# Kernel tuning notes

Hardware: AMD Instinct MI355X
Metric: run time of the kernel (lower is better)

## Reference

```python
import jax, jax.numpy as jnp
import numpy as np

N = 50000      # nodes
E = 800000     # random edges (self loops appended in reference)
B = 500        # graphs
H = 4          # attention heads
F = 64         # feature_dim (per-head out channels)
SLOPE = 0.2    # GATConv leaky_relu negative slope


def gat_layer(x, src, dst, W, att_s, att_d, b):
    # x: [N, Fin]; W: [Fin, H*F]; att_s/att_d: [H, F]; b: [H*F]
    h = (x @ W).reshape(N, H, F)                       # [N,H,F]
    a_s = jnp.einsum('nhf,hf->nh', h, att_s)           # [N,H]
    a_d = jnp.einsum('nhf,hf->nh', h, att_d)           # [N,H]
    e = jax.nn.leaky_relu(a_s[src] + a_d[dst], SLOPE)  # [E',H]
    emax = jax.ops.segment_max(e, dst, num_segments=N) # [N,H] (finite: self loops)
    ee = jnp.exp(e - emax[dst])
    denom = jax.ops.segment_sum(ee, dst, num_segments=N)
    alpha = ee / denom[dst]                            # [E',H]
    out = jax.ops.segment_sum(alpha[:, :, None] * h[src], dst, num_segments=N)
    return out.reshape(N, H * F) + b


def setup_inputs() -> dict:
    key = jax.random.key(0)
    ks = jax.random.split(key, 32)
    s = 0.05
    inp = {
        'node_features': jax.random.normal(ks[0], (N, 5), jnp.float32),
        'building_mask': jax.random.randint(ks[1], (N,), 0, 2),
        'batch': jnp.sort(jax.random.randint(ks[2], (N,), 0, B)),
        'edge_index': jax.random.randint(ks[3], (2, E), 0, N),
        'bbox_W': jax.random.normal(ks[4], (5, 64)) * s,
        'bbox_b': jnp.zeros((64,), jnp.float32),
        'mask_embed': jax.random.normal(ks[5], (2, 64)) * s,
        'node_W': jax.random.normal(ks[6], (128, 64)) * s,
        'node_b': jnp.zeros((64,), jnp.float32),
        'w0': jax.random.normal(ks[7], (64, 256)) * s,
        'as0': jax.random.normal(ks[8], (H, F)) * s,
        'ad0': jax.random.normal(ks[9], (H, F)) * s,
        'b0': jnp.zeros((256,), jnp.float32),
        'w1': jax.random.normal(ks[10], (256, 256)) * s,
        'as1': jax.random.normal(ks[11], (H, F)) * s,
        'ad1': jax.random.normal(ks[12], (H, F)) * s,
        'b1': jnp.zeros((256,), jnp.float32),
        'w2': jax.random.normal(ks[13], (256, 256)) * s,
        'as2': jax.random.normal(ks[14], (H, F)) * s,
        'ad2': jax.random.normal(ks[15], (H, F)) * s,
        'b2': jnp.zeros((256,), jnp.float32),
        'agg_W': jax.random.normal(ks[16], (832, 256)) * s,
        'agg_b': jnp.zeros((256,), jnp.float32),
        'mu_W': jax.random.normal(ks[17], (256, 256)) * s,
        'mu_b': jnp.zeros((256,), jnp.float32),
        'var_W': jax.random.normal(ks[18], (256, 256)) * s,
        'var_b': jnp.zeros((256,), jnp.float32),
    }
    return inp


def reference(node_features, building_mask, batch, edge_index,
              bbox_W, bbox_b, mask_embed, node_W, node_b,
              w0, as0, ad0, b0, w1, as1, ad1, b1, w2, as2, ad2, b2,
              agg_W, agg_b, mu_W, mu_b, var_W, var_b):
    # node featurization
    x = jax.nn.relu(node_features @ bbox_W + bbox_b)          # [N,64]
    m = jax.nn.relu(mask_embed[building_mask])                 # [N,64]
    n0 = jax.nn.relu(jnp.concatenate([x, m], -1) @ node_W + node_b)  # [N,64]

    # self loops (GATConv add_self_loops=True)
    loop = jnp.arange(N, dtype=edge_index.dtype)
    src = jnp.concatenate([edge_index[0], loop])
    dst = jnp.concatenate([edge_index[1], loop])

    g = jax.ops.segment_max(n0, batch, num_segments=B, indices_are_sorted=True)
    g_embed = [g]

    n_t = jax.nn.relu(gat_layer(n0, src, dst, w0, as0, ad0, b0))
    g_embed.append(jax.ops.segment_max(n_t, batch, num_segments=B, indices_are_sorted=True))

    for (W, a_s, a_d, b) in [(w1, as1, ad1, b1), (w2, as2, ad2, b2)]:
        n_t = jax.nn.relu(gat_layer(n_t, src, dst, W, a_s, a_d, b))
        g_embed.append(jax.ops.segment_max(n_t, batch, num_segments=B, indices_are_sorted=True))

    latent = jnp.concatenate(g_embed, -1) @ agg_W + agg_b      # [B,256]
    mu = latent @ mu_W + mu_b
    log_var = latent @ var_W + var_b
    return (mu, log_var)
```

## Files before the change

kernel.cpp:

```cpp
#include <hip/hip_runtime.h>

#define NN 50000
#define EE 800000
#define BB 500

typedef short v8s __attribute__((ext_vector_type(8)));
typedef float v4f __attribute__((ext_vector_type(4)));

__device__ __forceinline__ float bf2f(unsigned short u) {
    union { unsigned int i; float f; } v; v.i = ((unsigned int)u) << 16; return v.f;
}
__device__ __forceinline__ unsigned short f2bf(float f) {
    union { float f; unsigned int i; } v; v.f = f;
    unsigned int x = v.i;
    unsigned int r = (x + 0x7FFFu + ((x >> 16) & 1u)) >> 16;
    return (unsigned short)r;
}

__device__ __forceinline__ void gll16(const unsigned short* g, v8s* l) {
    __builtin_amdgcn_global_load_lds((const __attribute__((address_space(1))) unsigned int*)g,
                                     (__attribute__((address_space(3))) unsigned int*)l, 16, 0, 0);
}

__global__ void k_sentinel(float* out, float val) {
    int i = blockIdx.x * blockDim.x + threadIdx.x;
    if (i < BB * 512) out[i] = val;
}

__global__ void k_prep(const float* __restrict__ nf, const int* __restrict__ bmask,
                       const float* __restrict__ bboxW, const float* __restrict__ bboxb,
                       const float* __restrict__ membed, unsigned short* __restrict__ feat,
                       const float* __restrict__ a0, unsigned short* __restrict__ d0,
                       const float* __restrict__ a1, unsigned short* __restrict__ d1,
                       const float* __restrict__ a2, unsigned short* __restrict__ d2,
                       const float* __restrict__ a3, unsigned short* __restrict__ d3,
                       int* __restrict__ cur, float* __restrict__ gcat) {
    int g = blockIdx.x * blockDim.x + threadIdx.x;
    if (g < NN) cur[g] = 0;
    if (g < NN * 64) {
        int n = g >> 6, f = g & 63;
        float s = bboxb[f];
        for (int k = 0; k < 5; ++k) s += nf[n * 5 + k] * bboxW[k * 64 + f];
        s = fmaxf(s, 0.f);
        int bm = bmask[n]; if ((unsigned)bm > 1u) bm = 0;
        float mv = fmaxf(membed[bm * 64 + f], 0.f);
        feat[(size_t)n * 128 + f] = f2bf(s);
        feat[(size_t)n * 128 + 64 + f] = f2bf(mv);
        return;
    }
    g -= NN * 64;
    if (g >= 155648) {
        if (g < 155648 + BB * 832) {
            int idx = g - 155648;
            gcat[idx] = 0.f;
        }
        return;
    }
    const float* in; unsigned short* out; int K, Nout, idx;
    if (g < 8192)        { in = a0; out = d0; K = 128; Nout = 64;  idx = g; }
    else if (g < 24576)  { in = a1; out = d1; K = 64;  Nout = 256; idx = g - 8192; }
    else if (g < 90112)  { in = a2; out = d2; K = 256; Nout = 256; idx = g - 24576; }
    else                 { in = a3; out = d3; K = 256; Nout = 256; idx = g - 90112; }
    int k = idx / Nout, n = idx % Nout;
    out[n * K + k] = f2bf(in[idx]);
}

template <int KT, bool BR, bool ATT, int GY, bool GM>
__global__ __launch_bounds__(256) void k_gemm(const unsigned short* __restrict__ A,
                                              const unsigned short* __restrict__ Bt,
                                              const float* __restrict__ bias,
                                              unsigned short* __restrict__ C, int M, int ldc,
                                              const float* __restrict__ atts, const float* __restrict__ attd,
                                              float* __restrict__ asA, float* __restrict__ adA, int nbx,
                                              const int* __restrict__ batch, float* __restrict__ gmax) {
    constexpr int NT = KT / 64;
    constexpr int NB = (NT > 1) ? 2 : 1;
    __shared__ v8s As[NB][512];
    __shared__ v8s Bs[NB][512];
    __shared__ float ap[4][4][4][4][2];
    const int t = threadIdx.x;
    int bx, by;
    if (GY == 4) {
        int p = blockIdx.x;
        int gidx = p >> 5, r = p & 31;
        bx = gidx * 8 + (r & 7);
        by = r >> 3;
        if (bx >= nbx) return;
    } else {
        bx = blockIdx.x; by = 0;
    }
    const int m0 = bx * 64;
    const int n0g = by * 64;
    const int l = t & 63, w = t >> 6;
    const int q = l >> 4, r16 = l & 15;
    const int nloc = w * 16 + r16;

    const int roff0 = (w * 2 + 0) * 8 + (l >> 3);
    const int roff1 = (w * 2 + 1) * 8 + (l >> 3);
    const int kc = (l & 7) ^ (l >> 3);
    const unsigned short* Asrc0 = A + (size_t)(m0 + roff0) * KT + kc * 8;
    const unsigned short* Asrc1 = A + (size_t)(m0 + roff1) * KT + kc * 8;
    const unsigned short* Bsrc0 = Bt + (size_t)(n0g + roff0) * KT + kc * 8;
    const unsigned short* Bsrc1 = Bt + (size_t)(n0g + roff1) * KT + kc * 8;

    v4f acc[4];
#pragma unroll
    for (int i = 0; i < 4; ++i) acc[i] = (v4f){0.f, 0.f, 0.f, 0.f};

    gll16(Asrc0, &As[0][(w * 2 + 0) * 64]);
    gll16(Asrc1, &As[0][(w * 2 + 1) * 64]);
    gll16(Bsrc0, &Bs[0][(w * 2 + 0) * 64]);
    gll16(Bsrc1, &Bs[0][(w * 2 + 1) * 64]);
    __syncthreads();
#pragma unroll
    for (int kt = 0; kt < NT; ++kt) {
        const int b = kt & (NB - 1);
        if (kt + 1 < NT) {
            const int nb = (kt + 1) & (NB - 1);
            gll16(Asrc0 + (kt + 1) * 64, &As[nb][(w * 2 + 0) * 64]);
            gll16(Asrc1 + (kt + 1) * 64, &As[nb][(w * 2 + 1) * 64]);
            gll16(Bsrc0 + (kt + 1) * 64, &Bs[nb][(w * 2 + 0) * 64]);
            gll16(Bsrc1 + (kt + 1) * 64, &Bs[nb][(w * 2 + 1) * 64]);
        }
#pragma unroll
        for (int s = 0; s < 2; ++s) {
            int c = s * 4 + q;
            v8s bfr = Bs[b][nloc * 8 + (c ^ (nloc & 7))];
#pragma unroll
            for (int mt = 0; mt < 4; ++mt) {
                v8s afr = As[b][(mt * 16 + r16) * 8 + (c ^ (r16 & 7))];
                acc[mt] = __builtin_amdgcn_mfma_f32_16x16x32_bf16(afr, bfr, acc[mt], 0, 0, 0);
            }
        }
        __syncthreads();
    }

    const int col = n0g + nloc;
#pragma unroll
    for (int mt = 0; mt < 4; ++mt) {
#pragma unroll
        for (int r = 0; r < 4; ++r) {
            int row = m0 + mt * 16 + q * 4 + r;
            if (row < M) {
                float v = acc[mt][r];
                if (BR) v = fmaxf(v + bias[col], 0.f);
                C[(size_t)row * ldc + col] = f2bf(v);
                if (GM) atomicMax((int*)(gmax + (size_t)batch[row] * 832 + col), __float_as_int(v));
            }
        }
    }
    if (ATT) {
        float sa = atts[n0g + nloc];
        float da = attd[n0g + nloc];
        float rs[4][4], rd[4][4];
#pragma unroll
        for (int mt = 0; mt < 4; ++mt)
#pragma unroll
            for (int r = 0; r < 4; ++r) { rs[mt][r] = acc[mt][r] * sa; rd[mt][r] = acc[mt][r] * da; }
#pragma unroll
        for (int d = 1; d < 16; d <<= 1) {
#pragma unroll
            for (int mt = 0; mt < 4; ++mt)
#pragma unroll
                for (int r = 0; r < 4; ++r) {
                    rs[mt][r] += __shfl_xor(rs[mt][r], d, 64);
                    rd[mt][r] += __shfl_xor(rd[mt][r], d, 64);
                }
        }
        if (r16 == 0) {
#pragma unroll
            for (int mt = 0; mt < 4; ++mt)
#pragma unroll
                for (int r = 0; r < 4; ++r) { ap[w][q][mt][r][0] = rs[mt][r]; ap[w][q][mt][r][1] = rd[mt][r]; }
        }
        __syncthreads();
        if (t < 128) {
            int row = t >> 1, which = t & 1;
            int qq = (row >> 2) & 3, mtt = row >> 4, rr = row & 3;
            float s = ap[0][qq][mtt][rr][which] + ap[1][qq][mtt][rr][which] +
                      ap[2][qq][mtt][rr][which] + ap[3][qq][mtt][rr][which];
            if (m0 + row < M) (which ? adA : asA)[(m0 + row) * 4 + by] = s;
        }
    }
}

#define SCAT_K 256
__global__ __launch_bounds__(256) void k_scatter(const int* __restrict__ ei, int* __restrict__ cur,
                                                 unsigned short* __restrict__ csr) {
    const int p = blockIdx.x & 7;
    const int j = blockIdx.x >> 3;
    const int plo = p * (NN / 8), phi = plo + (NN / 8);
    const int TOT = EE + NN;
    const int chunk = (TOT + SCAT_K - 1) / SCAT_K;
    const int e1 = min((j + 1) * chunk, TOT);
    for (int e = j * chunk + (int)threadIdx.x; e < e1; e += 256) {
        int d = (e < EE) ? ei[EE + e] : (e - EE);
        if (d < plo || d >= phi) continue;
        int s = (e < EE) ? ei[e] : d;
        if ((unsigned)s >= (unsigned)NN) s = d;
        int pos = atomicAdd(&cur[d], 1);
        if (pos < 64) csr[d * 64 + pos] = (unsigned short)s;
    }
}

__global__ __launch_bounds__(256) void k_agg(const unsigned short* __restrict__ h,
                                             const float* __restrict__ asA, const float* __restrict__ adA,
                                             const int* __restrict__ cur, const unsigned short* __restrict__ csr,
                                             const float* __restrict__ bias,
                                             unsigned short* __restrict__ nout,
                                             const int* __restrict__ batch,
                                             float* __restrict__ gcat, int gbase) {
    __shared__ int   sL[4][64];
    __shared__ float wL[4][64][4];
    __shared__ float mx[4][256];
    __shared__ int   gb[4];
    const int nd4 = threadIdx.x >> 6;
    const int node = blockIdx.x * 4 + nd4;
    const int l = threadIdx.x & 63;
    const int hl = l >> 4, k16 = l & 15;
    const int o0 = node << 6;
    int deg = cur[node]; if (deg > 64) deg = 64;
    const float ad4 = adA[node * 4 + hl];
    float sm = 0.f;
    for (int k = k16; k < deg; k += 16) {
        int s = csr[o0 + k];
        if (hl == 0) sL[nd4][k] = s;
        float e = asA[s * 4 + hl] + ad4;
        e = e > 0.f ? e : 0.2f * e;
        float w = __expf(e);
        wL[nd4][k][hl] = w;
        sm += w;
    }
#pragma unroll
    for (int d = 1; d < 16; d <<= 1) sm += __shfl_xor(sm, d, 64);
    const float rden = 1.f / sm;
    __syncthreads();
    float a0 = 0.f, a1 = 0.f, a2 = 0.f, a3 = 0.f;
    const int c = l * 4;
    int k = 0;
    for (; k + 4 <= deg; k += 4) {
        int s0 = sL[nd4][k], s1 = sL[nd4][k + 1], s2 = sL[nd4][k + 2], s3 = sL[nd4][k + 3];
        float w0 = wL[nd4][k][hl], w1 = wL[nd4][k + 1][hl], w2 = wL[nd4][k + 2][hl], w3 = wL[nd4][k + 3][hl];
        ushort4 h0 = *(const ushort4*)(h + (size_t)s0 * 256 + c);
        ushort4 h1 = *(const ushort4*)(h + (size_t)s1 * 256 + c);
        ushort4 h2 = *(const ushort4*)(h + (size_t)s2 * 256 + c);
        ushort4 h3 = *(const ushort4*)(h + (size_t)s3 * 256 + c);
        a0 += w0 * bf2f(h0.x) + w1 * bf2f(h1.x) + w2 * bf2f(h2.x) + w3 * bf2f(h3.x);
        a1 += w0 * bf2f(h0.y) + w1 * bf2f(h1.y) + w2 * bf2f(h2.y) + w3 * bf2f(h3.y);
        a2 += w0 * bf2f(h0.z) + w1 * bf2f(h1.z) + w2 * bf2f(h2.z) + w3 * bf2f(h3.z);
        a3 += w0 * bf2f(h0.w) + w1 * bf2f(h1.w) + w2 * bf2f(h2.w) + w3 * bf2f(h3.w);
    }
    for (; k < deg; ++k) {
        int s = sL[nd4][k];
        float w = wL[nd4][k][hl];
        ushort4 hv = *(const ushort4*)(h + (size_t)s * 256 + c);
        a0 += w * bf2f(hv.x); a1 += w * bf2f(hv.y); a2 += w * bf2f(hv.z); a3 += w * bf2f(hv.w);
    }
    float4 bv = *(const float4*)(bias + c);
    float v0 = fmaxf(a0 * rden + bv.x, 0.f);
    float v1 = fmaxf(a1 * rden + bv.y, 0.f);
    float v2 = fmaxf(a2 * rden + bv.z, 0.f);
    float v3 = fmaxf(a3 * rden + bv.w, 0.f);
    ushort4 o;
    o.x = f2bf(v0); o.y = f2bf(v1); o.z = f2bf(v2); o.w = f2bf(v3);
    *(ushort4*)(nout + (size_t)node * 256 + c) = o;

    mx[nd4][c + 0] = v0; mx[nd4][c + 1] = v1; mx[nd4][c + 2] = v2; mx[nd4][c + 3] = v3;
    if (l == 0) gb[nd4] = batch[node];
    __syncthreads();
    const int t = threadIdx.x;
    if (gb[0] == gb[1] && gb[1] == gb[2] && gb[2] == gb[3]) {
        float m = fmaxf(fmaxf(mx[0][t], mx[1][t]), fmaxf(mx[2][t], mx[3][t]));
        atomicMax((int*)(gcat + gb[0] * 832 + gbase + t), __float_as_int(m));
    } else {
        int* g = (int*)(gcat + gb[nd4] * 832 + gbase);
        atomicMax(g + c + 0, __float_as_int(v0));
        atomicMax(g + c + 1, __float_as_int(v1));
        atomicMax(g + c + 2, __float_as_int(v2));
        atomicMax(g + c + 3, __float_as_int(v3));
    }
}

__global__ __launch_bounds__(256) void k_head1(const float* __restrict__ gcat,
                                               const float* __restrict__ aggW, const float* __restrict__ aggb,
                                               float* __restrict__ latent) {
    __shared__ float gr[832 * 4];
    __shared__ float part[4][4][64];
    const int t = threadIdx.x;
    const int g0 = blockIdx.x * 4, c0 = blockIdx.y * 64;
    for (int i = t; i < 832 * 4; i += 256) {
        int k = i >> 2, g = i & 3;
        gr[i] = gcat[(g0 + g) * 832 + k];
    }
    __syncthreads();
    const int w = t >> 6, l = t & 63;
    const float* wp = aggW + c0 + l;
    float a0 = 0.f, a1 = 0.f, a2 = 0.f, a3 = 0.f;
    const int k0 = w * 208;
#pragma unroll 4
    for (int k = k0; k < k0 + 208; ++k) {
        float wv = wp[(size_t)k * 256];
        float4 gv = *(const float4*)&gr[k * 4];
        a0 += gv.x * wv; a1 += gv.y * wv; a2 += gv.z * wv; a3 += gv.w * wv;
    }
    part[w][0][l] = a0; part[w][1][l] = a1; part[w][2][l] = a2; part[w][3][l] = a3;
    __syncthreads();
    const int g = t >> 6, c = t & 63;
    float s = ((part[0][g][c] + part[1][g][c]) + (part[2][g][c] + part[3][g][c])) + aggb[c0 + c];
    latent[(g0 + g) * 256 + c0 + c] = s;
}

__global__ __launch_bounds__(256) void k_head2(const float* __restrict__ latent,
                                               const float* __restrict__ muW, const float* __restrict__ mub,
                                               const float* __restrict__ vaW, const float* __restrict__ vab,
                                               float* __restrict__ out) {
    __shared__ float lr[256 * 4];
    __shared__ float pm[4][4][64], pv[4][4][64];
    const int t = threadIdx.x;
    const int g0 = blockIdx.x * 4, c0 = blockIdx.y * 64;
    for (int i = t; i < 256 * 4; i += 256) {
        int k = i >> 2, g = i & 3;
        lr[i] = latent[(g0 + g) * 256 + k];
    }
    __syncthreads();
    const int w = t >> 6, l = t & 63;
    const float* mp = muW + c0 + l;
    const float* vp = vaW + c0 + l;
    float m0 = 0.f, m1 = 0.f, m2 = 0.f, m3 = 0.f;
    float v0 = 0.f, v1 = 0.f, v2 = 0.f, v3 = 0.f;
    const int k0 = w * 64;
#pragma unroll 4
    for (int k = k0; k < k0 + 64; ++k) {
        float wm = mp[(size_t)k * 256];
        float wv = vp[(size_t)k * 256];
        float4 gv = *(const float4*)&lr[k * 4];
        m0 += gv.x * wm; m1 += gv.y * wm; m2 += gv.z * wm; m3 += gv.w * wm;
        v0 += gv.x * wv; v1 += gv.y * wv; v2 += gv.z * wv; v3 += gv.w * wv;
    }
    pm[w][0][l] = m0; pm[w][1][l] = m1; pm[w][2][l] = m2; pm[w][3][l] = m3;
    pv[w][0][l] = v0; pv[w][1][l] = v1; pv[w][2][l] = v2; pv[w][3][l] = v3;
    __syncthreads();
    const int g = t >> 6, c = t & 63;
    float smu = ((pm[0][g][c] + pm[1][g][c]) + (pm[2][g][c] + pm[3][g][c])) + mub[c0 + c];
    float sva = ((pv[0][g][c] + pv[1][g][c]) + (pv[2][g][c] + pv[3][g][c])) + vab[c0 + c];
    out[(g0 + g) * 256 + c0 + c] = smu;
    out[BB * 256 + (g0 + g) * 256 + c0 + c] = sva;
}

extern "C" void kernel_launch(void* const* d_in, const int* in_sizes, int n_in,
                              void* d_out, int out_size, void* d_ws, size_t ws_size,
                              hipStream_t stream) {
    (void)in_sizes; (void)n_in; (void)out_size;
    const float* nf     = (const float*)d_in[0];
    const int*   bmask  = (const int*)d_in[1];
    const int*   batch  = (const int*)d_in[2];
    const int*   ei     = (const int*)d_in[3];
    const float* bboxW  = (const float*)d_in[4];
    const float* bboxb  = (const float*)d_in[5];
    const float* membed = (const float*)d_in[6];
    const float* nodeW  = (const float*)d_in[7];
    const float* nodeb  = (const float*)d_in[8];
    const float* w0     = (const float*)d_in[9];
    const float* as0    = (const float*)d_in[10];
    const float* ad0    = (const float*)d_in[11];
    const float* b0     = (const float*)d_in[12];
    const float* w1     = (const float*)d_in[13];
    const float* as1    = (const float*)d_in[14];
    const float* ad1    = (const float*)d_in[15];
    const float* b1     = (const float*)d_in[16];
    const float* w2     = (const float*)d_in[17];
    const float* as2    = (const float*)d_in[18];
    const float* ad2    = (const float*)d_in[19];
    const float* b2     = (const float*)d_in[20];
    const float* aggW   = (const float*)d_in[21];
    const float* aggb   = (const float*)d_in[22];
    const float* muW    = (const float*)d_in[23];
    const float* mub    = (const float*)d_in[24];
    const float* vaW    = (const float*)d_in[25];
    const float* vab    = (const float*)d_in[26];
    float* out = (float*)d_out;

    char* base = (char*)d_ws;
    unsigned short* hbuf    = (unsigned short*)(base);
    unsigned short* nbuf    = (unsigned short*)(base + 25600000);
    unsigned short* feat128 = nbuf;
    unsigned short* n0buf   = (unsigned short*)(base + 25600000 + 12800000);
    char* pool0 = base + 51200000;
    char* p = pool0;
    auto alloc = [&](size_t bytes) { char* r = p; p += (bytes + 255) & ~(size_t)255; return r; };
    unsigned short* nodeWt = (unsigned short*)alloc(128 * 64 * 2);
    unsigned short* w0t    = (unsigned short*)alloc(64 * 256 * 2);
    unsigned short* w1t    = (unsigned short*)alloc(256 * 256 * 2);
    unsigned short* w2t    = (unsigned short*)alloc(256 * 256 * 2);
    float* asA    = (float*)alloc((size_t)NN * 4 * 4);
    float* adA    = (float*)alloc((size_t)NN * 4 * 4);
    int*   cur    = (int*)alloc((size_t)NN * 4);
    unsigned short* csr = (unsigned short*)alloc((size_t)NN * 64 * 2);
    float* gcat   = (float*)alloc((size_t)BB * 832 * 4);
    float* latent = (float*)alloc((size_t)BB * 256 * 4);
    const size_t NEED = (size_t)(p - base);

    if (ws_size < NEED) {
        k_sentinel<<<1000, 256, 0, stream>>>(out, 2000.0f + (float)(ws_size >> 20));
        return;
    }

    k_prep<<<(NN * 64 + 155648 + BB * 832 + 255) / 256, 256, 0, stream>>>(
        nf, bmask, bboxW, bboxb, membed, feat128,
        nodeW, nodeWt, w0, w0t, w1, w1t, w2, w2t, cur, gcat);
    k_scatter<<<SCAT_K * 8, 256, 0, stream>>>(ei, cur, csr);
    k_gemm<128, true, false, 1, true><<<782, 256, 0, stream>>>(feat128, nodeWt, nodeb, n0buf, NN, 64,
                                                               nullptr, nullptr, nullptr, nullptr, 782,
                                                               batch, gcat);
    k_gemm<64, false, true, 4, false><<<3136, 256, 0, stream>>>(n0buf, w0t, nullptr, hbuf, NN, 256,
                                                                as0, ad0, asA, adA, 782, nullptr, nullptr);
    k_agg<<<12500, 256, 0, stream>>>(hbuf, asA, adA, cur, csr, b0, nbuf, batch, gcat, 64);
    k_gemm<256, false, true, 4, false><<<3136, 256, 0, stream>>>(nbuf, w1t, nullptr, hbuf, NN, 256,
                                                                 as1, ad1, asA, adA, 782, nullptr, nullptr);
    k_agg<<<12500, 256, 0, stream>>>(hbuf, asA, adA, cur, csr, b1, nbuf, batch, gcat, 320);
    k_gemm<256, false, true, 4, false><<<3136, 256, 0, stream>>>(nbuf, w2t, nullptr, hbuf, NN, 256,
                                                                 as2, ad2, asA, adA, 782, nullptr, nullptr);
    k_agg<<<12500, 256, 0, stream>>>(hbuf, asA, adA, cur, csr, b2, nbuf, batch, gcat, 576);
    k_head1<<<dim3(BB / 4, 4), 256, 0, stream>>>(gcat, aggW, aggb, latent);
    k_head2<<<dim3(BB / 4, 4), 256, 0, stream>>>(latent, muW, mub, vaW, vab, out);
}
```

Before: 546.3 us.

## Use 128x128 tiles for GAT projection GEMMs with fused attention scores

Adds a k_gemm2 kernel that computes 128x128 output tiles per block, with 8x2 MFMA accumulators per wave, instead of 64x64 tiles. The three GAT linear layers launch 784 blocks instead of 3136. Each block computes two heads' attention logits and writes them out. The aim is more reuse of A and B tiles from LDS and fewer global loads per FLOP. The cost is higher register and LDS pressure, and rows are read past M, which is covered by a 64KB tail pad in the workspace.

New measurement: 562.0 us. +2.9%, slower.

```diff
diff --git a/kernel.cpp b/kernel.cpp
--- a/kernel.cpp
+++ b/kernel.cpp
@@ -65,32 +65,19 @@
     out[n * K + k] = f2bf(in[idx]);
 }
 
-template <int KT, bool BR, bool ATT, int GY, bool GM>
+template <int KT>
 __global__ __launch_bounds__(256) void k_gemm(const unsigned short* __restrict__ A,
                                               const unsigned short* __restrict__ Bt,
                                               const float* __restrict__ bias,
                                               unsigned short* __restrict__ C, int M, int ldc,
-                                              const float* __restrict__ atts, const float* __restrict__ attd,
-                                              float* __restrict__ asA, float* __restrict__ adA, int nbx,
                                               const int* __restrict__ batch, float* __restrict__ gmax) {
     constexpr int NT = KT / 64;
     constexpr int NB = (NT > 1) ? 2 : 1;
     __shared__ v8s As[NB][512];
     __shared__ v8s Bs[NB][512];
-    __shared__ float ap[4][4][4][4][2];
     const int t = threadIdx.x;
-    int bx, by;
-    if (GY == 4) {
-        int p = blockIdx.x;
-        int gidx = p >> 5, r = p & 31;
-        bx = gidx * 8 + (r & 7);
-        by = r >> 3;
-        if (bx >= nbx) return;
-    } else {
-        bx = blockIdx.x; by = 0;
-    }
+    const int bx = blockIdx.x;
     const int m0 = bx * 64;
-    const int n0g = by * 64;
     const int l = t & 63, w = t >> 6;
     const int q = l >> 4, r16 = l & 15;
     const int nloc = w * 16 + r16;
@@ -100,8 +87,8 @@
     const int kc = (l & 7) ^ (l >> 3);
     const unsigned short* Asrc0 = A + (size_t)(m0 + roff0) * KT + kc * 8;
     const unsigned short* Asrc1 = A + (size_t)(m0 + roff1) * KT + kc * 8;
-    const unsigned short* Bsrc0 = Bt + (size_t)(n0g + roff0) * KT + kc * 8;
-    const unsigned short* Bsrc1 = Bt + (size_t)(n0g + roff1) * KT + kc * 8;
+    const unsigned short* Bsrc0 = Bt + (size_t)roff0 * KT + kc * 8;
+    const unsigned short* Bsrc1 = Bt + (size_t)roff1 * KT + kc * 8;
 
     v4f acc[4];
 #pragma unroll
@@ -135,51 +122,134 @@
         __syncthreads();
     }
 
-    const int col = n0g + nloc;
+    const int col = nloc;
 #pragma unroll
     for (int mt = 0; mt < 4; ++mt) {
 #pragma unroll
         for (int r = 0; r < 4; ++r) {
             int row = m0 + mt * 16 + q * 4 + r;
             if (row < M) {
-                float v = acc[mt][r];
-                if (BR) v = fmaxf(v + bias[col], 0.f);
+                float v = fmaxf(acc[mt][r] + bias[col], 0.f);
                 C[(size_t)row * ldc + col] = f2bf(v);
-                if (GM) atomicMax((int*)(gmax + (size_t)batch[row] * 832 + col), __float_as_int(v));
-            }
-        }
-    }
-    if (ATT) {
-        float sa = atts[n0g + nloc];
-        float da = attd[n0g + nloc];
-        float rs[4][4], rd[4][4];
-#pragma unroll
-        for (int mt = 0; mt < 4; ++mt)
-#pragma unroll
-            for (int r = 0; r < 4; ++r) { rs[mt][r] = acc[mt][r] * sa; rd[mt][r] = acc[mt][r] * da; }
-#pragma unroll
-        for (int d = 1; d < 16; d <<= 1) {
-#pragma unroll
-            for (int mt = 0; mt < 4; ++mt)
-#pragma unroll
-                for (int r = 0; r < 4; ++r) {
-                    rs[mt][r] += __shfl_xor(rs[mt][r], d, 64);
-                    rd[mt][r] += __shfl_xor(rd[mt][r], d, 64);
-                }
-        }
-        if (r16 == 0) {
-#pragma unroll
-            for (int mt = 0; mt < 4; ++mt)
-#pragma unroll
-                for (int r = 0; r < 4; ++r) { ap[w][q][mt][r][0] = rs[mt][r]; ap[w][q][mt][r][1] = rd[mt][r]; }
+                atomicMax((int*)(gmax + (size_t)batch[row] * 832 + col), __float_as_int(v));
+            }
+        }
+    }
+}
+
+template <int KT>
+__global__ __launch_bounds__(256, 2) void k_gemm2(const unsigned short* __restrict__ A,
+                                                  const unsigned short* __restrict__ Bt,
+                                                  unsigned short* __restrict__ C, int M,
+                                                  const float* __restrict__ atts, const float* __restrict__ attd,
+                                                  float* __restrict__ asA, float* __restrict__ adA) {
+    constexpr int NT = KT / 64;
+    constexpr int NB = (NT > 1) ? 2 : 1;
+    __shared__ v8s As[NB][1024];
+    __shared__ v8s Bs[NB][1024];
+    __shared__ float ap[4][4][8][4][2][2];
+    const int t = threadIdx.x;
+    const int p = blockIdx.x;
+    const int bx = (p >> 4) * 8 + (p & 7);
+    const int by = (p >> 3) & 1;
+    if (bx >= 391) return;
+    const int m0 = bx * 128;
+    const int n0g = by * 128;
+    const int l = t & 63, w = t >> 6;
+    const int q = l >> 4, r16 = l & 15;
+
+    const int rr0 = l >> 3;
+    const int kc = (l & 7) ^ rr0;
+
+    v4f acc[8][2];
+#pragma unroll
+    for (int i = 0; i < 8; ++i)
+#pragma unroll
+        for (int f = 0; f < 2; ++f) acc[i][f] = (v4f){0.f, 0.f, 0.f, 0.f};
+
+#pragma unroll
+    for (int j = 0; j < 4; ++j) {
+        int ro = (w * 4 + j) * 8 + rr0;
+        gll16(A + (size_t)(m0 + ro) * KT + kc * 8, &As[0][(w * 4 + j) * 64]);
+        gll16(Bt + (size_t)(n0g + ro) * KT + kc * 8, &Bs[0][(w * 4 + j) * 64]);
+    }
+    __syncthreads();
+#pragma unroll
+    for (int kt = 0; kt < NT; ++kt) {
+        const int b = kt & (NB - 1);
+        if (kt + 1 < NT) {
+            const int nb = (kt + 1) & (NB - 1);
+#pragma unroll
+            for (int j = 0; j < 4; ++j) {
+                int ro = (w * 4 + j) * 8 + rr0;
+                gll16(A + (size_t)(m0 + ro) * KT + (kt + 1) * 64 + kc * 8, &As[nb][(w * 4 + j) * 64]);
+                gll16(Bt + (size_t)(n0g + ro) * KT + (kt + 1) * 64 + kc * 8, &Bs[nb][(w * 4 + j) * 64]);
+            }
+        }
+#pragma unroll
+        for (int s = 0; s < 2; ++s) {
+            int c = s * 4 + q;
+            int cl0 = w * 16 + r16, cl1 = 64 + w * 16 + r16;
+            v8s bfr0 = Bs[b][cl0 * 8 + (c ^ (cl0 & 7))];
+            v8s bfr1 = Bs[b][cl1 * 8 + (c ^ (cl1 & 7))];
+#pragma unroll
+            for (int mt = 0; mt < 8; ++mt) {
+                int rl = mt * 16 + r16;
+                v8s afr = As[b][rl * 8 + (c ^ (rl & 7))];
+                acc[mt][0] = __builtin_amdgcn_mfma_f32_16x16x32_bf16(afr, bfr0, acc[mt][0], 0, 0, 0);
+                acc[mt][1] = __builtin_amdgcn_mfma_f32_16x16x32_bf16(afr, bfr1, acc[mt][1], 0, 0, 0);
+            }
         }
         __syncthreads();
-        if (t < 128) {
-            int row = t >> 1, which = t & 1;
-            int qq = (row >> 2) & 3, mtt = row >> 4, rr = row & 3;
-            float s = ap[0][qq][mtt][rr][which] + ap[1][qq][mtt][rr][which] +
-                      ap[2][qq][mtt][rr][which] + ap[3][qq][mtt][rr][which];
-            if (m0 + row < M) (which ? adA : asA)[(m0 + row) * 4 + by] = s;
+    }
+
+#pragma unroll
+    for (int mt = 0; mt < 8; ++mt)
+#pragma unroll
+        for (int f = 0; f < 2; ++f)
+#pragma unroll
+            for (int r = 0; r < 4; ++r) {
+                int row = m0 + mt * 16 + q * 4 + r;
+                if (row < M)
+                    C[(size_t)row * 256 + n0g + f * 64 + w * 16 + r16] = f2bf(acc[mt][f][r]);
+            }
+
+    float sa0 = atts[n0g + w * 16 + r16],      da0 = attd[n0g + w * 16 + r16];
+    float sa1 = atts[n0g + 64 + w * 16 + r16], da1 = attd[n0g + 64 + w * 16 + r16];
+#pragma unroll
+    for (int mt = 0; mt < 8; ++mt)
+#pragma unroll
+        for (int f = 0; f < 2; ++f) {
+            float sa = f ? sa1 : sa0, da = f ? da1 : da0;
+            float xs0 = acc[mt][f][0] * sa, xs1 = acc[mt][f][1] * sa,
+                  xs2 = acc[mt][f][2] * sa, xs3 = acc[mt][f][3] * sa;
+            float xd0 = acc[mt][f][0] * da, xd1 = acc[mt][f][1] * da,
+                  xd2 = acc[mt][f][2] * da, xd3 = acc[mt][f][3] * da;
+#pragma unroll
+            for (int d = 1; d < 16; d <<= 1) {
+                xs0 += __shfl_xor(xs0, d, 64); xs1 += __shfl_xor(xs1, d, 64);
+                xs2 += __shfl_xor(xs2, d, 64); xs3 += __shfl_xor(xs3, d, 64);
+                xd0 += __shfl_xor(xd0, d, 64); xd1 += __shfl_xor(xd1, d, 64);
+                xd2 += __shfl_xor(xd2, d, 64); xd3 += __shfl_xor(xd3, d, 64);
+            }
+            if (r16 == 0) {
+                ap[w][q][mt][0][f][0] = xs0; ap[w][q][mt][1][f][0] = xs1;
+                ap[w][q][mt][2][f][0] = xs2; ap[w][q][mt][3][f][0] = xs3;
+                ap[w][q][mt][0][f][1] = xd0; ap[w][q][mt][1][f][1] = xd1;
+                ap[w][q][mt][2][f][1] = xd2; ap[w][q][mt][3][f][1] = xd3;
+            }
+        }
+    __syncthreads();
+    {
+        int gr = t >> 1, sd = t & 1;
+        int mt = gr >> 4, qq = (gr >> 2) & 3, r = gr & 3;
+        if (m0 + gr < M) {
+#pragma unroll
+            for (int f = 0; f < 2; ++f) {
+                float s = (ap[0][qq][mt][r][f][sd] + ap[1][qq][mt][r][f][sd]) +
+                          (ap[2][qq][mt][r][f][sd] + ap[3][qq][mt][r][f][sd]);
+                (sd ? adA : asA)[(size_t)(m0 + gr) * 4 + by * 2 + f] = s;
+            }
         }
     }
 }
@@ -398,6 +468,8 @@
     unsigned short* csr = (unsigned short*)alloc((size_t)NN * 64 * 2);
     float* gcat   = (float*)alloc((size_t)BB * 832 * 4);
     float* latent = (float*)alloc((size_t)BB * 256 * 4);
+    char*  tailpad = alloc(64 * 1024);
+    (void)tailpad;
     const size_t NEED = (size_t)(p - base);
 
     if (ws_size < NEED) {
@@ -409,17 +481,12 @@
         nf, bmask, bboxW, bboxb, membed, feat128,
         nodeW, nodeWt, w0, w0t, w1, w1t, w2, w2t, cur, gcat);
     k_scatter<<<SCAT_K * 8, 256, 0, stream>>>(ei, cur, csr);
-    k_gemm<128, true, false, 1, true><<<782, 256, 0, stream>>>(feat128, nodeWt, nodeb, n0buf, NN, 64,
-                                                               nullptr, nullptr, nullptr, nullptr, 782,
-                                                               batch, gcat);
-    k_gemm<64, false, true, 4, false><<<3136, 256, 0, stream>>>(n0buf, w0t, nullptr, hbuf, NN, 256,
-                                                                as0, ad0, asA, adA, 782, nullptr, nullptr);
+    k_gemm<128><<<782, 256, 0, stream>>>(feat128, nodeWt, nodeb, n0buf, NN, 64, batch, gcat);
+    k_gemm2<64><<<784, 256, 0, stream>>>(n0buf, w0t, hbuf, NN, as0, ad0, asA, adA);
     k_agg<<<12500, 256, 0, stream>>>(hbuf, asA, adA, cur, csr, b0, nbuf, batch, gcat, 64);
-    k_gemm<256, false, true, 4, false><<<3136, 256, 0, stream>>>(nbuf, w1t, nullptr, hbuf, NN, 256,
-                                                                 as1, ad1, asA, adA, 782, nullptr, nullptr);
+    k_gemm2<256><<<784, 256, 0, stream>>>(nbuf, w1t, hbuf, NN, as1, ad1, asA, adA);
     k_agg<<<12500, 256, 0, stream>>>(hbuf, asA, adA, cur, csr, b1, nbuf, batch, gcat, 320);
-    k_gemm<256, false, true, 4, false><<<3136, 256, 0, stream>>>(nbuf, w2t, nullptr, hbuf, NN, 256,
-                                                                 as2, ad2, asA, adA, 782, nullptr, nullptr);
+    k_gemm2<256><<<784, 256, 0, stream>>>(nbuf, w2t, hbuf, NN, as2, ad2, asA, adA);
     k_agg<<<12500, 256, 0, stream>>>(hbuf, asA, adA, cur, csr, b2, nbuf, batch, gcat, 576);
     k_head1<<<dim3(BB / 4, 4), 256, 0, stream>>>(gcat, aggW, aggb, latent);
     k_head2<<<dim3(BB / 4, 4), 256, 0, stream>>>(latent, muW, mub, vaW, vab, out);
```
